# Kernel tuning notes

Measured on AMD Instinct MI355X. Metric: run time of the kernel, lower is better.

Reference implementation:

```python
import jax, jax.numpy as jnp
import numpy as np

NEG_SLOPE = 0.2  # PyG GATConv default leaky_relu slope


def segment_softmax(logits, seg, num_segments):
    # logits: [E, H], seg: [E] destination node ids
    m = jax.ops.segment_max(logits, seg, num_segments=num_segments)
    m = jnp.where(jnp.isfinite(m), m, 0.0)  # empty segments
    e = jnp.exp(logits - m[seg])
    s = jax.ops.segment_sum(e, seg, num_segments=num_segments)
    return e / (s[seg] + 1e-16)


def gat_conv(x, src, dst, W, att_src, att_dst, bias, heads, out_ch, concat, num_nodes):
    # x: [N, F_in], W: [F_in, heads*out_ch], att_*: [heads, out_ch]
    h = (x @ W).reshape(num_nodes, heads, out_ch)            # [N, H, C]
    a_src = jnp.sum(h * att_src, axis=-1)                    # [N, H]
    a_dst = jnp.sum(h * att_dst, axis=-1)                    # [N, H]
    logits = jax.nn.leaky_relu(a_src[src] + a_dst[dst], NEG_SLOPE)  # [E, H]
    alpha = segment_softmax(logits, dst, num_nodes)          # [E, H]
    msg = h[src] * alpha[..., None]                          # [E, H, C]
    out = jax.ops.segment_sum(msg, dst, num_segments=num_nodes)  # [N, H, C]
    out = out.reshape(num_nodes, heads * out_ch) if concat else out.mean(axis=1)
    return out + bias


def setup_inputs() -> dict:
    key = jax.random.key(0)
    ks = jax.random.split(key, 12)
    N, E = 50000, 800000
    F_in, Hd, H, F_out = 256, 128, 2, 64

    def glorot(k, shape):
        fan = shape[0] + shape[-1]
        return jax.random.normal(k, shape, dtype=jnp.float32) * jnp.sqrt(2.0 / fan)

    x = jax.random.normal(ks[0], (N, F_in), dtype=jnp.float32)
    edge_index = jax.random.randint(ks[1], (2, E), 0, N, dtype=jnp.int32)
    return {
        "x": x,
        "edge_index": edge_index,
        "W1": glorot(ks[2], (F_in, H * Hd)),
        "att_src1": glorot(ks[3], (H, Hd)),
        "att_dst1": glorot(ks[4], (H, Hd)),
        "b1": jnp.zeros((H * Hd,), dtype=jnp.float32),
        "W2": glorot(ks[5], (H * Hd, F_out)),
        "att_src2": glorot(ks[6], (1, F_out)),
        "att_dst2": glorot(ks[7], (1, F_out)),
        "b2": jnp.zeros((F_out,), dtype=jnp.float32),
    }


def reference(x, edge_index, W1, att_src1, att_dst1, b1, W2, att_src2, att_dst2, b2):
    N = x.shape[0]
    # PyG GATConv default: add self loops
    ar = jnp.arange(N, dtype=edge_index.dtype)
    src = jnp.concatenate([edge_index[0], ar])
    dst = jnp.concatenate([edge_index[1], ar])
    # dropout layers are identity in eval mode
    h = gat_conv(x, src, dst, W1, att_src1, att_dst1, b1,
                 heads=2, out_ch=128, concat=True, num_nodes=N)
    h = jax.nn.elu(h)
    out = gat_conv(h, src, dst, W2, att_src2, att_dst2, b2,
                   heads=1, out_ch=64, concat=False, num_nodes=N)
    return jax.nn.log_softmax(out, axis=1)
```

## Files before the change

### kernel.cpp

```cpp
#include <hip/hip_runtime.h>
#include <hip/hip_bf16.h>

typedef unsigned short u16;
typedef short bf8_t __attribute__((ext_vector_type(8)));
typedef float f32x4 __attribute__((ext_vector_type(4)));

__device__ inline u16 f2bf(float f) {
  unsigned u = __float_as_uint(f);
  u += 0x7FFFu + ((u >> 16) & 1u);
  return (u16)(u >> 16);
}
__device__ inline float bf2f(u16 h) { return __uint_as_float(((unsigned)h) << 16); }
__device__ inline float bflo(unsigned u) { return __uint_as_float(u << 16); }
__device__ inline float bfhi(unsigned u) { return __uint_as_float(u & 0xffff0000u); }

__global__ void prep_kernel(const int* __restrict__ ei, int E, int N,
                            int* __restrict__ counts,
                            const float* __restrict__ W1, const float* __restrict__ W2,
                            u16* __restrict__ W1T, u16* __restrict__ W2T, int nbc) {
  if ((int)blockIdx.x < nbc) {
    int e = blockIdx.x * 256 + threadIdx.x;
    int Et = E + N;
    if (e < Et) {
      int d = (e < E) ? ei[E + e] : (e - E);
      atomicAdd(&counts[d], 1);
    }
  } else {
    int idx = (blockIdx.x - nbc) * 256 + threadIdx.x;
    if (idx < 256 * 256) {
      int m = idx / 256, k = idx % 256;
      W1T[idx] = f2bf(W1[(size_t)k * 256 + m]);
    } else if (idx < 256 * 256 + 64 * 256) {
      int i = idx - 256 * 256;
      int m = i / 256, k = i % 256;
      W2T[i] = f2bf(W2[(size_t)k * 64 + m]);
    }
  }
}

template<int BM, int BN, int BK, int WM, int WN, bool AF32, int EPI>
__global__ __launch_bounds__(256) void mfma_gemm(const void* __restrict__ Ap,
                                                 const u16* __restrict__ Bt,
                                                 u16* __restrict__ C,
                                                 const float* __restrict__ att_s,
                                                 const float* __restrict__ att_d,
                                                 float* __restrict__ a_s,
                                                 float* __restrict__ a_d,
                                                 int N, int K) {
  constexpr int PAD = 8;
  __shared__ u16 As[BM][BK + PAD];
  __shared__ u16 Bs[BN][BK + PAD];
  const int tid = threadIdx.x;
  const int row0 = blockIdx.x * BM;
  const int w = tid >> 6, lane = tid & 63;
  const int wr = (w / (BN / WN)) * WM;
  const int wc = (w % (BN / WN)) * WN;
  constexpr int MF = WM / 16, NF = WN / 16;
  constexpr int CPR = BK / 8;
  f32x4 acc[MF][NF] = {};

  for (int k0 = 0; k0 < K; k0 += BK) {
    constexpr int ACH = BM * CPR;
#pragma unroll
    for (int c = 0; c < ACH; c += 256) {
      int cc = c + tid;
      int r = cc / CPR, kc = cc % CPR;
      int row = row0 + r;
      if (AF32) {
        const float* A = (const float*)Ap;
        float4 v0 = make_float4(0.f, 0.f, 0.f, 0.f), v1 = v0;
        if (row < N) {
          const float* p = A + (size_t)row * K + k0 + kc * 8;
          v0 = *(const float4*)p;
          v1 = *(const float4*)(p + 4);
        }
        union { __hip_bfloat162 h[4]; uint4 u; } cv;
        cv.h[0] = __float22bfloat162_rn(make_float2(v0.x, v0.y));
        cv.h[1] = __float22bfloat162_rn(make_float2(v0.z, v0.w));
        cv.h[2] = __float22bfloat162_rn(make_float2(v1.x, v1.y));
        cv.h[3] = __float22bfloat162_rn(make_float2(v1.z, v1.w));
        *(uint4*)&As[r][kc * 8] = cv.u;
      } else {
        const u16* A = (const u16*)Ap;
        uint4 v = make_uint4(0, 0, 0, 0);
        if (row < N) v = *(const uint4*)(A + (size_t)row * K + k0 + kc * 8);
        *(uint4*)&As[r][kc * 8] = v;
      }
    }
    constexpr int BCH = BN * CPR;
#pragma unroll
    for (int c = 0; c < BCH; c += 256) {
      int cc = c + tid;
      int r = cc / CPR, kc = cc % CPR;
      *(uint4*)&Bs[r][kc * 8] = *(const uint4*)(Bt + (size_t)r * K + k0 + kc * 8);
    }
    __syncthreads();
    const int lr = lane & 15, lk = (lane >> 4) * 8;
#pragma unroll
    for (int kk = 0; kk < BK; kk += 32) {
      bf8_t a[MF], b[NF];
#pragma unroll
      for (int mi = 0; mi < MF; ++mi) a[mi] = *(bf8_t*)&As[wr + mi * 16 + lr][kk + lk];
#pragma unroll
      for (int ni = 0; ni < NF; ++ni) b[ni] = *(bf8_t*)&Bs[wc + ni * 16 + lr][kk + lk];
#pragma unroll
      for (int mi = 0; mi < MF; ++mi)
#pragma unroll
        for (int ni = 0; ni < NF; ++ni)
          acc[mi][ni] = __builtin_amdgcn_mfma_f32_16x16x32_bf16(a[mi], b[ni], acc[mi][ni], 0, 0, 0);
    }
    __syncthreads();
  }
#pragma unroll
  for (int mi = 0; mi < MF; ++mi)
#pragma unroll
    for (int ni = 0; ni < NF; ++ni)
#pragma unroll
      for (int r = 0; r < 4; ++r) {
        int row = row0 + wr + mi * 16 + (lane >> 4) * 4 + r;
        int col = wc + ni * 16 + (lane & 15);
        if (row < N) C[(size_t)row * BN + col] = f2bf(acc[mi][ni][r]);
      }

  if (EPI == 1) {
    __shared__ float sm_s[4][64];
    __shared__ float sm_d[4][64];
    float asl[NF], adl[NF];
#pragma unroll
    for (int ni = 0; ni < NF; ++ni) {
      asl[ni] = att_s[wc + ni * 16 + (lane & 15)];
      adl[ni] = att_d[wc + ni * 16 + (lane & 15)];
    }
#pragma unroll
    for (int mi = 0; mi < MF; ++mi)
#pragma unroll
      for (int r = 0; r < 4; ++r) {
        float ps = 0.f, pd = 0.f;
#pragma unroll
        for (int ni = 0; ni < NF; ++ni) {
          float c = acc[mi][ni][r];
          ps += c * asl[ni];
          pd += c * adl[ni];
        }
#pragma unroll
        for (int o = 1; o < 16; o <<= 1) {
          ps += __shfl_xor(ps, o);
          pd += __shfl_xor(pd, o);
        }
        if ((lane & 15) == 0) {
          int row = mi * 16 + (lane >> 4) * 4 + r;
          sm_s[w][row] = ps;
          sm_d[w][row] = pd;
        }
      }
    __syncthreads();
    if (tid < 128) {
      int row = tid & 63, head = tid >> 6;
      int grow = row0 + row;
      if (grow < N) {
        a_s[grow * 2 + head] = sm_s[head * 2 + 0][row] + sm_s[head * 2 + 1][row];
        a_d[grow * 2 + head] = sm_d[head * 2 + 0][row] + sm_d[head * 2 + 1][row];
      }
    }
  } else if (EPI == 2) {
    float asl[NF], adl[NF];
#pragma unroll
    for (int ni = 0; ni < NF; ++ni) {
      asl[ni] = att_s[ni * 16 + (lane & 15)];
      adl[ni] = att_d[ni * 16 + (lane & 15)];
    }
#pragma unroll
    for (int mi = 0; mi < MF; ++mi)
#pragma unroll
      for (int r = 0; r < 4; ++r) {
        float ps = 0.f, pd = 0.f;
#pragma unroll
        for (int ni = 0; ni < NF; ++ni) {
          float c = acc[mi][ni][r];
          ps += c * asl[ni];
          pd += c * adl[ni];
        }
#pragma unroll
        for (int o = 1; o < 16; o <<= 1) {
          ps += __shfl_xor(ps, o);
          pd += __shfl_xor(pd, o);
        }
        int row = row0 + wr + mi * 16 + (lane >> 4) * 4 + r;
        if ((lane & 15) == 0 && row < N) {
          a_s[row] = ps;
          a_d[row] = pd;
        }
      }
  }
}

__global__ void block_scan_kernel(const int* __restrict__ counts, int* __restrict__ offsets,
                                  int* __restrict__ bsums, int N) {
  __shared__ int sm[256];
  int tid = threadIdx.x;
  int gid = blockIdx.x * 256 + tid;
  int v = (gid < N) ? counts[gid] : 0;
  int val = v;
  sm[tid] = val;
  __syncthreads();
  for (int off = 1; off < 256; off <<= 1) {
    int o = (tid >= off) ? sm[tid - off] : 0;
    __syncthreads();
    val += o;
    sm[tid] = val;
    __syncthreads();
  }
  if (gid < N) offsets[gid] = val - v;
  if (tid == 255) bsums[blockIdx.x] = val;
}

__global__ void scan_sums_kernel(int* __restrict__ bsums, int* __restrict__ offsets,
                                 int nb, int N) {
  __shared__ int sm[1024];
  int tid = threadIdx.x;
  int v = (tid < nb) ? bsums[tid] : 0;
  int val = v;
  sm[tid] = val;
  __syncthreads();
  for (int off = 1; off < 1024; off <<= 1) {
    int o = (tid >= off) ? sm[tid - off] : 0;
    __syncthreads();
    val += o;
    sm[tid] = val;
    __syncthreads();
  }
  if (tid < nb) bsums[tid] = val - v;
  if (tid == 1023) offsets[N] = val;
}

__global__ void add_base_kernel(int* __restrict__ offsets, int* __restrict__ cursor,
                                const int* __restrict__ bsums, int N) {
  int gid = blockIdx.x * 256 + threadIdx.x;
  if (gid >= N) return;
  int o = offsets[gid] + bsums[blockIdx.x];
  offsets[gid] = o;
  cursor[gid] = o;
}

__global__ void scatter_kernel(const int* __restrict__ ei, int E, int N,
                               int* __restrict__ cursor, int* __restrict__ csr_src) {
  int e = blockIdx.x * blockDim.x + threadIdx.x;
  int Et = E + N;
  if (e >= Et) return;
  int s, d;
  if (e < E) { s = ei[e]; d = ei[E + e]; }
  else       { s = d = e - E; }
  int pos = atomicAdd(&cursor[d], 1);
  csr_src[pos] = s;
}

__global__ void agg1_kernel(const u16* __restrict__ H1, const int* __restrict__ offsets,
                            const int* __restrict__ csr_src,
                            const float* __restrict__ a_src, const float* __restrict__ a_dst,
                            const float* __restrict__ b1, u16* __restrict__ out, int N) {
  __shared__ int4 meta[4][64];
  int wv = threadIdx.x >> 6;
  int lane = threadIdx.x & 63;
  int node = blockIdx.x * 4 + wv;
  if (node >= N) return;
  int off = offsets[node];
  int deg = offsets[node + 1] - off;
  float ad0 = a_dst[node * 2 + 0];
  float ad1 = a_dst[node * 2 + 1];
  bool hi = lane >= 32;
  const char* H1c = (const char*)H1;
  const unsigned loff = (unsigned)(lane * 8);
  float4 acc = make_float4(0.f, 0.f, 0.f, 0.f);
  float den = 0.f;
  const int4* mw = meta[wv];

  auto proc = [&](int4 m) {
    float w = hi ? __int_as_float(m.z) : __int_as_float(m.y);
    uint2 u = *(const uint2*)(H1c + (((unsigned)m.x << 9) + loff));
    den += w;
    acc.x += w * bflo(u.x);
    acc.y += w * bfhi(u.x);
    acc.z += w * bflo(u.y);
    acc.w += w * bfhi(u.y);
  };

  for (int base = 0; base < deg; base += 64) {
    int i = base + lane;
    if (i < deg) {
      int s = csr_src[off + i];
      float l0 = a_src[s * 2 + 0] + ad0;
      float l1 = a_src[s * 2 + 1] + ad1;
      l0 = l0 > 0.f ? l0 : 0.2f * l0;
      l1 = l1 > 0.f ? l1 : 0.2f * l1;
      meta[wv][lane] = make_int4(s, __float_as_int(__expf(l0)), __float_as_int(__expf(l1)), 0);
    }
    int cnt = min(64, deg - base);
    int j = 0;
    for (; j + 4 <= cnt; j += 4) {
      int4 m0 = mw[j], m1 = mw[j + 1], m2 = mw[j + 2], m3 = mw[j + 3];
      proc(m0); proc(m1); proc(m2); proc(m3);
    }
    for (; j < cnt; ++j) proc(mw[j]);
  }
  float inv = 1.f / (den + 1e-16f);
  float4 bb = *(const float4*)(b1 + lane * 4);
  float o0 = acc.x * inv + bb.x;
  float o1 = acc.y * inv + bb.y;
  float o2 = acc.z * inv + bb.z;
  float o3 = acc.w * inv + bb.w;
  o0 = o0 > 0.f ? o0 : expm1f(o0);
  o1 = o1 > 0.f ? o1 : expm1f(o1);
  o2 = o2 > 0.f ? o2 : expm1f(o2);
  o3 = o3 > 0.f ? o3 : expm1f(o3);
  uint2 ov;
  ov.x = (unsigned)f2bf(o0) | ((unsigned)f2bf(o1) << 16);
  ov.y = (unsigned)f2bf(o2) | ((unsigned)f2bf(o3) << 16);
  *(uint2*)(out + (size_t)node * 256 + lane * 4) = ov;
}

__global__ void agg2_kernel(const u16* __restrict__ H2, const int* __restrict__ offsets,
                            const int* __restrict__ csr_src,
                            const float* __restrict__ a_src, const float* __restrict__ a_dst,
                            const float* __restrict__ b2, float* __restrict__ out, int N) {
  __shared__ int2 meta[4][64];
  int wv = threadIdx.x >> 6;
  int lane = threadIdx.x & 63;
  int node = blockIdx.x * 4 + wv;
  if (node >= N) return;
  int off = offsets[node];
  int deg = offsets[node + 1] - off;
  float ad = a_dst[node];
  const int grp = lane >> 3;
  const int l3 = lane & 7;
  const char* H2c = (const char*)H2;
  const unsigned loff = (unsigned)(l3 * 16);
  float acc[8] = {0.f, 0.f, 0.f, 0.f, 0.f, 0.f, 0.f, 0.f};
  float den = 0.f;
  const int2* mw = meta[wv];

  auto proc = [&](int jj) {
    int2 m = mw[jj];
    float w = __int_as_float(m.y);
    uint4 u = *(const uint4*)(H2c + (((unsigned)m.x << 7) + loff));
    den += w;
    acc[0] += w * bflo(u.x); acc[1] += w * bfhi(u.x);
    acc[2] += w * bflo(u.y); acc[3] += w * bfhi(u.y);
    acc[4] += w * bflo(u.z); acc[5] += w * bfhi(u.z);
    acc[6] += w * bflo(u.w); acc[7] += w * bfhi(u.w);
  };

  for (int base = 0; base < deg; base += 64) {
    int i = base + lane;
    if (i < deg) {
      int s = csr_src[off + i];
      float l = a_src[s] + ad;
      l = l > 0.f ? l : 0.2f * l;
      meta[wv][lane] = make_int2(s, __float_as_int(__expf(l)));
    }
    int cnt = min(64, deg - base);
    int j = 0;
    for (; j + 16 <= cnt; j += 16) { proc(j + grp); proc(j + 8 + grp); }
    for (; j + 8 <= cnt; j += 8) proc(j + grp);
    int r = cnt - j;
    if (r > 0 && grp < r) proc(j + grp);
  }
#pragma unroll
  for (int k = 0; k < 8; ++k) {
    acc[k] += __shfl_xor(acc[k], 8);
    acc[k] += __shfl_xor(acc[k], 16);
    acc[k] += __shfl_xor(acc[k], 32);
  }
  den += __shfl_xor(den, 8);
  den += __shfl_xor(den, 16);
  den += __shfl_xor(den, 32);

  float inv = 1.f / (den + 1e-16f);
  float4 b01 = *(const float4*)(b2 + l3 * 8);
  float4 b23 = *(const float4*)(b2 + l3 * 8 + 4);
  float bb[8] = {b01.x, b01.y, b01.z, b01.w, b23.x, b23.y, b23.z, b23.w};
  float v[8];
#pragma unroll
  for (int k = 0; k < 8; ++k) v[k] = acc[k] * inv + bb[k];
  float m = v[0];
#pragma unroll
  for (int k = 1; k < 8; ++k) m = fmaxf(m, v[k]);
  m = fmaxf(m, __shfl_xor(m, 1));
  m = fmaxf(m, __shfl_xor(m, 2));
  m = fmaxf(m, __shfl_xor(m, 4));
  float sum = 0.f;
#pragma unroll
  for (int k = 0; k < 8; ++k) sum += __expf(v[k] - m);
  sum += __shfl_xor(sum, 1);
  sum += __shfl_xor(sum, 2);
  sum += __shfl_xor(sum, 4);
  float ls = m + logf(sum);
  if (lane < 8) {
    float4 o0 = make_float4(v[0] - ls, v[1] - ls, v[2] - ls, v[3] - ls);
    float4 o1 = make_float4(v[4] - ls, v[5] - ls, v[6] - ls, v[7] - ls);
    *(float4*)(out + (size_t)node * 64 + l3 * 8) = o0;
    *(float4*)(out + (size_t)node * 64 + l3 * 8 + 4) = o1;
  }
}

extern "C" void kernel_launch(void* const* d_in, const int* in_sizes, int n_in,
                              void* d_out, int out_size, void* d_ws, size_t ws_size,
                              hipStream_t stream) {
  const float* x   = (const float*)d_in[0];
  const int*   ei  = (const int*)d_in[1];
  const float* W1  = (const float*)d_in[2];
  const float* as1 = (const float*)d_in[3];
  const float* ad1 = (const float*)d_in[4];
  const float* b1  = (const float*)d_in[5];
  const float* W2  = (const float*)d_in[6];
  const float* as2 = (const float*)d_in[7];
  const float* ad2 = (const float*)d_in[8];
  const float* b2  = (const float*)d_in[9];
  float* out = (float*)d_out;

  const int N  = in_sizes[0] / 256;
  const int E  = in_sizes[1] / 2;
  const int Et = E + N;
  const int nb = (N + 255) / 256;
  const int nbc = (Et + 255) / 256;
  const int nbt = (256 * 256 + 64 * 256 + 255) / 256;

  char* p = (char*)d_ws;
  auto alloc = [&](size_t bytes) -> char* {
    char* r = p;
    p += (bytes + 255) & ~(size_t)255;
    return r;
  };
  u16* H1b     = (u16*)alloc((size_t)N * 256 * 2);
  u16* h1act   = (u16*)alloc((size_t)N * 256 * 2);
  u16* H2b     = (u16*)alloc((size_t)N * 64 * 2);
  u16* W1T     = (u16*)alloc((size_t)256 * 256 * 2);
  u16* W2T     = (u16*)alloc((size_t)64 * 256 * 2);
  float* a_src1 = (float*)alloc((size_t)N * 2 * 4);
  float* a_dst1 = (float*)alloc((size_t)N * 2 * 4);
  float* a_src2 = (float*)alloc((size_t)N * 4);
  float* a_dst2 = (float*)alloc((size_t)N * 4);
  int* counts   = (int*)alloc((size_t)N * 4);
  int* offsets  = (int*)alloc((size_t)(N + 1) * 4);
  int* cursor   = (int*)alloc((size_t)N * 4);
  int* bsums    = (int*)alloc((size_t)1024 * 4);
  int* csr_src  = (int*)alloc((size_t)Et * 4);

  const int tb = 256;

  hipMemsetAsync(counts, 0, (size_t)N * 4, stream);
  prep_kernel<<<nbc + nbt, tb, 0, stream>>>(ei, E, N, counts, W1, W2, W1T, W2T, nbc);
  block_scan_kernel<<<nb, 256, 0, stream>>>(counts, offsets, bsums, N);
  scan_sums_kernel<<<1, 1024, 0, stream>>>(bsums, offsets, nb, N);
  add_base_kernel<<<nb, 256, 0, stream>>>(offsets, cursor, bsums, N);
  scatter_kernel<<<(Et + tb - 1) / tb, tb, 0, stream>>>(ei, E, N, cursor, csr_src);

  mfma_gemm<64, 256, 64, 64, 64, true, 1><<<(N + 63) / 64, 256, 0, stream>>>(
      x, W1T, H1b, as1, ad1, a_src1, a_dst1, N, 256);
  agg1_kernel<<<(N + 3) / 4, 256, 0, stream>>>(H1b, offsets, csr_src, a_src1, a_dst1, b1,
                                               h1act, N);

  mfma_gemm<128, 64, 64, 32, 64, false, 2><<<(N + 127) / 128, 256, 0, stream>>>(
      h1act, W2T, H2b, as2, ad2, a_src2, a_dst2, N, 256);
  agg2_kernel<<<(N + 3) / 4, 256, 0, stream>>>(H2b, offsets, csr_src, a_src2, a_dst2, b2,
                                               out, N);
}
```

Baseline: 234.9 us.

## Fuse CSR construction into one cooperative kernel and shrink GEMM K-tile

Replaces the memset, the prep kernel, the three scan kernels and the scatter kernel with one cooperative kernel. It uses grid-wide syncs between the count, scan, base-add and scatter phases, with weight transposition folded into the first phase. The goal is to remove several launches and their inter-kernel gaps, at the price of grid.sync overhead and only 256 persistent blocks doing the edge atomics. The scan assumes N fits in 256x256 threads. Both GEMMs also drop BK from 64 to 32, trading fewer LDS bytes and possibly higher occupancy for more K-loop iterations.

Result: slower. 367.3 us (+56.4%).

```diff
diff --git a/kernel.cpp b/kernel.cpp
--- a/kernel.cpp
+++ b/kernel.cpp
@@ -1,5 +1,8 @@
 #include <hip/hip_runtime.h>
 #include <hip/hip_bf16.h>
+#include <hip/hip_cooperative_groups.h>
+
+namespace cg = cooperative_groups;
 
 typedef unsigned short u16;
 typedef short bf8_t __attribute__((ext_vector_type(8)));
@@ -14,27 +17,81 @@
 __device__ inline float bflo(unsigned u) { return __uint_as_float(u << 16); }
 __device__ inline float bfhi(unsigned u) { return __uint_as_float(u & 0xffff0000u); }
 
-__global__ void prep_kernel(const int* __restrict__ ei, int E, int N,
-                            int* __restrict__ counts,
-                            const float* __restrict__ W1, const float* __restrict__ W2,
-                            u16* __restrict__ W1T, u16* __restrict__ W2T, int nbc) {
-  if ((int)blockIdx.x < nbc) {
-    int e = blockIdx.x * 256 + threadIdx.x;
-    int Et = E + N;
-    if (e < Et) {
-      int d = (e < E) ? ei[E + e] : (e - E);
-      atomicAdd(&counts[d], 1);
-    }
-  } else {
-    int idx = (blockIdx.x - nbc) * 256 + threadIdx.x;
-    if (idx < 256 * 256) {
-      int m = idx / 256, k = idx % 256;
-      W1T[idx] = f2bf(W1[(size_t)k * 256 + m]);
-    } else if (idx < 256 * 256 + 64 * 256) {
-      int i = idx - 256 * 256;
-      int m = i / 256, k = i % 256;
-      W2T[i] = f2bf(W2[(size_t)k * 64 + m]);
-    }
+__global__ void csr_build_kernel(const int* __restrict__ ei, int E, int N,
+                                 const float* __restrict__ W1, const float* __restrict__ W2,
+                                 u16* __restrict__ W1T, u16* __restrict__ W2T,
+                                 int* __restrict__ counts, int* __restrict__ offsets,
+                                 int* __restrict__ cursor, int* __restrict__ bsums,
+                                 int* __restrict__ csr_src) {
+  cg::grid_group grid = cg::this_grid();
+  __shared__ int sm[256];
+  const int tid = threadIdx.x, bid = blockIdx.x;
+  const int gsz = gridDim.x * 256;
+  const int g = bid * 256 + tid;
+  const int Et = E + N;
+
+  for (int i = g; i < N; i += gsz) counts[i] = 0;
+  for (int i = g; i < 256 * 256; i += gsz) {
+    int m = i >> 8, k = i & 255;
+    W1T[i] = f2bf(W1[k * 256 + m]);
+  }
+  for (int i = g; i < 64 * 256; i += gsz) {
+    int m = i >> 8, k = i & 255;
+    W2T[i] = f2bf(W2[k * 64 + m]);
+  }
+  grid.sync();
+
+  for (int e = g; e < Et; e += gsz) {
+    int d = (e < E) ? ei[E + e] : (e - E);
+    atomicAdd(&counts[d], 1);
+  }
+  grid.sync();
+
+  int v = (g < N) ? counts[g] : 0;
+  int val = v;
+  sm[tid] = val;
+  __syncthreads();
+  for (int off = 1; off < 256; off <<= 1) {
+    int o = (tid >= off) ? sm[tid - off] : 0;
+    __syncthreads();
+    val += o;
+    sm[tid] = val;
+    __syncthreads();
+  }
+  if (g < N) offsets[g] = val - v;
+  if (tid == 255) bsums[bid] = val;
+  grid.sync();
+
+  if (bid == 0) {
+    int b = bsums[tid];
+    int bv = b;
+    sm[tid] = bv;
+    __syncthreads();
+    for (int off = 1; off < 256; off <<= 1) {
+      int o = (tid >= off) ? sm[tid - off] : 0;
+      __syncthreads();
+      bv += o;
+      sm[tid] = bv;
+      __syncthreads();
+    }
+    bsums[tid] = bv - b;
+    if (tid == 255) offsets[N] = bv;
+  }
+  grid.sync();
+
+  if (g < N) {
+    int o = offsets[g] + bsums[bid];
+    offsets[g] = o;
+    cursor[g] = o;
+  }
+  grid.sync();
+
+  for (int e = g; e < Et; e += gsz) {
+    int s, d;
+    if (e < E) { s = ei[e]; d = ei[E + e]; }
+    else       { s = d = e - E; }
+    int pos = atomicAdd(&cursor[d], 1);
+    csr_src[pos] = s;
   }
 }
 
@@ -194,66 +251,6 @@
   }
 }
 
-__global__ void block_scan_kernel(const int* __restrict__ counts, int* __restrict__ offsets,
-                                  int* __restrict__ bsums, int N) {
-  __shared__ int sm[256];
-  int tid = threadIdx.x;
-  int gid = blockIdx.x * 256 + tid;
-  int v = (gid < N) ? counts[gid] : 0;
-  int val = v;
-  sm[tid] = val;
-  __syncthreads();
-  for (int off = 1; off < 256; off <<= 1) {
-    int o = (tid >= off) ? sm[tid - off] : 0;
-    __syncthreads();
-    val += o;
-    sm[tid] = val;
-    __syncthreads();
-  }
-  if (gid < N) offsets[gid] = val - v;
-  if (tid == 255) bsums[blockIdx.x] = val;
-}
-
-__global__ void scan_sums_kernel(int* __restrict__ bsums, int* __restrict__ offsets,
-                                 int nb, int N) {
-  __shared__ int sm[1024];
-  int tid = threadIdx.x;
-  int v = (tid < nb) ? bsums[tid] : 0;
-  int val = v;
-  sm[tid] = val;
-  __syncthreads();
-  for (int off = 1; off < 1024; off <<= 1) {
-    int o = (tid >= off) ? sm[tid - off] : 0;
-    __syncthreads();
-    val += o;
-    sm[tid] = val;
-    __syncthreads();
-  }
-  if (tid < nb) bsums[tid] = val - v;
-  if (tid == 1023) offsets[N] = val;
-}
-
-__global__ void add_base_kernel(int* __restrict__ offsets, int* __restrict__ cursor,
-                                const int* __restrict__ bsums, int N) {
-  int gid = blockIdx.x * 256 + threadIdx.x;
-  if (gid >= N) return;
-  int o = offsets[gid] + bsums[blockIdx.x];
-  offsets[gid] = o;
-  cursor[gid] = o;
-}
-
-__global__ void scatter_kernel(const int* __restrict__ ei, int E, int N,
-                               int* __restrict__ cursor, int* __restrict__ csr_src) {
-  int e = blockIdx.x * blockDim.x + threadIdx.x;
-  int Et = E + N;
-  if (e >= Et) return;
-  int s, d;
-  if (e < E) { s = ei[e]; d = ei[E + e]; }
-  else       { s = d = e - E; }
-  int pos = atomicAdd(&cursor[d], 1);
-  csr_src[pos] = s;
-}
-
 __global__ void agg1_kernel(const u16* __restrict__ H1, const int* __restrict__ offsets,
                             const int* __restrict__ csr_src,
                             const float* __restrict__ a_src, const float* __restrict__ a_dst,
@@ -417,12 +414,9 @@
   const float* b2  = (const float*)d_in[9];
   float* out = (float*)d_out;
 
-  const int N  = in_sizes[0] / 256;
-  const int E  = in_sizes[1] / 2;
+  int N  = in_sizes[0] / 256;
+  int E  = in_sizes[1] / 2;
   const int Et = E + N;
-  const int nb = (N + 255) / 256;
-  const int nbc = (Et + 255) / 256;
-  const int nbt = (256 * 256 + 64 * 256 + 255) / 256;
 
   char* p = (char*)d_ws;
   auto alloc = [&](size_t bytes) -> char* {
@@ -445,21 +439,20 @@
   int* bsums    = (int*)alloc((size_t)1024 * 4);
   int* csr_src  = (int*)alloc((size_t)Et * 4);
 
-  const int tb = 256;
-
-  hipMemsetAsync(counts, 0, (size_t)N * 4, stream);
-  prep_kernel<<<nbc + nbt, tb, 0, stream>>>(ei, E, N, counts, W1, W2, W1T, W2T, nbc);
-  block_scan_kernel<<<nb, 256, 0, stream>>>(counts, offsets, bsums, N);
-  scan_sums_kernel<<<1, 1024, 0, stream>>>(bsums, offsets, nb, N);
-  add_base_kernel<<<nb, 256, 0, stream>>>(offsets, cursor, bsums, N);
-  scatter_kernel<<<(Et + tb - 1) / tb, tb, 0, stream>>>(ei, E, N, cursor, csr_src);
-
-  mfma_gemm<64, 256, 64, 64, 64, true, 1><<<(N + 63) / 64, 256, 0, stream>>>(
+  {
+    void* args[] = {(void*)&ei, (void*)&E, (void*)&N, (void*)&W1, (void*)&W2,
+                    (void*)&W1T, (void*)&W2T, (void*)&counts, (void*)&offsets,
+                    (void*)&cursor, (void*)&bsums, (void*)&csr_src};
+    hipLaunchCooperativeKernel((void*)csr_build_kernel, dim3(256), dim3(256),
+                               args, 0, stream);
+  }
+
+  mfma_gemm<64, 256, 32, 64, 64, true, 1><<<(N + 63) / 64, 256, 0, stream>>>(
       x, W1T, H1b, as1, ad1, a_src1, a_dst1, N, 256);
   agg1_kernel<<<(N + 3) / 4, 256, 0, stream>>>(H1b, offsets, csr_src, a_src1, a_dst1, b1,
                                                h1act, N);
 
-  mfma_gemm<128, 64, 64, 32, 64, false, 2><<<(N + 127) / 128, 256, 0, stream>>>(
+  mfma_gemm<128, 64, 32, 32, 64, false, 2><<<(N + 127) / 128, 256, 0, stream>>>(
       h1act, W2T, H2b, as2, ad2, a_src2, a_dst2, N, 256);
   agg2_kernel<<<(N + 3) / 4, 256, 0, stream>>>(H2b, offsets, csr_src, a_src2, a_dst2, b2,
                                                out, N);
```

## Fuse scan into decoupled-lookback kernel and merge CSR scatter into GEMM1 launch

Applied to the files above, without the earlier changes.

Replaces the three-kernel prefix scan with a single-pass decoupled-lookback scan that also initializes cursors. The CSR scatter now runs as extra blocks appended to the first GEMM launch, so that work overlaps with the matrix multiply. GEMM BK shrinks from 64 to 32, which changes shared-memory footprint and loop count. The aim is fewer launches and less serialization. The cost is spin-waiting in the scan, which relies on earlier blocks being scheduled first.

Result: slower. 276.8 us (+17.9%).

```diff
diff --git a/kernel.cpp b/kernel.cpp
--- a/kernel.cpp
+++ b/kernel.cpp
@@ -28,14 +28,66 @@
   } else {
     int idx = (blockIdx.x - nbc) * 256 + threadIdx.x;
     if (idx < 256 * 256) {
-      int m = idx / 256, k = idx % 256;
-      W1T[idx] = f2bf(W1[(size_t)k * 256 + m]);
+      int m = idx >> 8, k = idx & 255;
+      W1T[idx] = f2bf(W1[k * 256 + m]);
     } else if (idx < 256 * 256 + 64 * 256) {
       int i = idx - 256 * 256;
-      int m = i / 256, k = i % 256;
-      W2T[i] = f2bf(W2[(size_t)k * 64 + m]);
-    }
-  }
+      int m = i >> 8, k = i & 255;
+      W2T[i] = f2bf(W2[k * 64 + m]);
+    }
+  }
+}
+
+__global__ void scan_kernel(const int* __restrict__ counts, int* __restrict__ offsets,
+                            int* __restrict__ cursor,
+                            unsigned long long* __restrict__ bstate, int N, int nb) {
+  __shared__ int sm[256];
+  __shared__ int base_sh;
+  const int tid = threadIdx.x, bid = blockIdx.x;
+  const int gid = bid * 256 + tid;
+  int v = (gid < N) ? counts[gid] : 0;
+  int val = v;
+  sm[tid] = val;
+  __syncthreads();
+  for (int off = 1; off < 256; off <<= 1) {
+    int o = (tid >= off) ? sm[tid - off] : 0;
+    __syncthreads();
+    val += o;
+    sm[tid] = val;
+    __syncthreads();
+  }
+  int total = sm[255];
+  if (tid == 0) {
+    if (bid == 0) {
+      __hip_atomic_store(&bstate[0], ((unsigned long long)(unsigned)total << 32) | 2ull,
+                         __ATOMIC_RELEASE, __HIP_MEMORY_SCOPE_AGENT);
+      base_sh = 0;
+    } else {
+      __hip_atomic_store(&bstate[bid], ((unsigned long long)(unsigned)total << 32) | 1ull,
+                         __ATOMIC_RELEASE, __HIP_MEMORY_SCOPE_AGENT);
+      int base = 0;
+      for (int pb = bid - 1; pb >= 0; --pb) {
+        unsigned long long st;
+        do {
+          st = __hip_atomic_load(&bstate[pb], __ATOMIC_ACQUIRE, __HIP_MEMORY_SCOPE_AGENT);
+        } while ((st & 3ull) == 0ull);
+        base += (int)(unsigned)(st >> 32);
+        if ((st & 3ull) == 2ull) break;
+      }
+      __hip_atomic_store(&bstate[bid],
+                         ((unsigned long long)(unsigned)(base + total) << 32) | 2ull,
+                         __ATOMIC_RELEASE, __HIP_MEMORY_SCOPE_AGENT);
+      base_sh = base;
+    }
+  }
+  __syncthreads();
+  int base = base_sh;
+  if (gid < N) {
+    int o = base + val - v;
+    offsets[gid] = o;
+    cursor[gid] = o;
+  }
+  if (bid == nb - 1 && tid == 255) offsets[N] = base + total;
 }
 
 template<int BM, int BN, int BK, int WM, int WN, bool AF32, int EPI>
@@ -46,7 +98,24 @@
                                                  const float* __restrict__ att_d,
                                                  float* __restrict__ a_s,
                                                  float* __restrict__ a_d,
-                                                 int N, int K) {
+                                                 int N, int K,
+                                                 const int* __restrict__ ei, int E,
+                                                 int* __restrict__ cursor,
+                                                 int* __restrict__ csr_src,
+                                                 int gemmBlocks) {
+  if (EPI == 1 && (int)blockIdx.x >= gemmBlocks) {
+    int e = ((int)blockIdx.x - gemmBlocks) * 256 + (int)threadIdx.x;
+    int Et = E + N;
+    if (e < Et) {
+      int s, d;
+      if (e < E) { s = ei[e]; d = ei[E + e]; }
+      else       { s = d = e - E; }
+      int pos = atomicAdd(&cursor[d], 1);
+      csr_src[pos] = s;
+    }
+    return;
+  }
+
   constexpr int PAD = 8;
   __shared__ u16 As[BM][BK + PAD];
   __shared__ u16 Bs[BN][BK + PAD];
@@ -96,19 +165,16 @@
     }
     __syncthreads();
     const int lr = lane & 15, lk = (lane >> 4) * 8;
-#pragma unroll
-    for (int kk = 0; kk < BK; kk += 32) {
-      bf8_t a[MF], b[NF];
-#pragma unroll
-      for (int mi = 0; mi < MF; ++mi) a[mi] = *(bf8_t*)&As[wr + mi * 16 + lr][kk + lk];
-#pragma unroll
-      for (int ni = 0; ni < NF; ++ni) b[ni] = *(bf8_t*)&Bs[wc + ni * 16 + lr][kk + lk];
-#pragma unroll
-      for (int mi = 0; mi < MF; ++mi)
-#pragma unroll
-        for (int ni = 0; ni < NF; ++ni)
-          acc[mi][ni] = __builtin_amdgcn_mfma_f32_16x16x32_bf16(a[mi], b[ni], acc[mi][ni], 0, 0, 0);
-    }
+    bf8_t a[MF], b[NF];
+#pragma unroll
+    for (int mi = 0; mi < MF; ++mi) a[mi] = *(bf8_t*)&As[wr + mi * 16 + lr][lk];
+#pragma unroll
+    for (int ni = 0; ni < NF; ++ni) b[ni] = *(bf8_t*)&Bs[wc + ni * 16 + lr][lk];
+#pragma unroll
+    for (int mi = 0; mi < MF; ++mi)
+#pragma unroll
+      for (int ni = 0; ni < NF; ++ni)
+        acc[mi][ni] = __builtin_amdgcn_mfma_f32_16x16x32_bf16(a[mi], b[ni], acc[mi][ni], 0, 0, 0);
     __syncthreads();
   }
 #pragma unroll
@@ -192,66 +258,6 @@
         }
       }
   }
-}
-
-__global__ void block_scan_kernel(const int* __restrict__ counts, int* __restrict__ offsets,
-                                  int* __restrict__ bsums, int N) {
-  __shared__ int sm[256];
-  int tid = threadIdx.x;
-  int gid = blockIdx.x * 256 + tid;
-  int v = (gid < N) ? counts[gid] : 0;
-  int val = v;
-  sm[tid] = val;
-  __syncthreads();
-  for (int off = 1; off < 256; off <<= 1) {
-    int o = (tid >= off) ? sm[tid - off] : 0;
-    __syncthreads();
-    val += o;
-    sm[tid] = val;
-    __syncthreads();
-  }
-  if (gid < N) offsets[gid] = val - v;
-  if (tid == 255) bsums[blockIdx.x] = val;
-}
-
-__global__ void scan_sums_kernel(int* __restrict__ bsums, int* __restrict__ offsets,
-                                 int nb, int N) {
-  __shared__ int sm[1024];
-  int tid = threadIdx.x;
-  int v = (tid < nb) ? bsums[tid] : 0;
-  int val = v;
-  sm[tid] = val;
-  __syncthreads();
-  for (int off = 1; off < 1024; off <<= 1) {
-    int o = (tid >= off) ? sm[tid - off] : 0;
-    __syncthreads();
-    val += o;
-    sm[tid] = val;
-    __syncthreads();
-  }
-  if (tid < nb) bsums[tid] = val - v;
-  if (tid == 1023) offsets[N] = val;
-}
-
-__global__ void add_base_kernel(int* __restrict__ offsets, int* __restrict__ cursor,
-                                const int* __restrict__ bsums, int N) {
-  int gid = blockIdx.x * 256 + threadIdx.x;
-  if (gid >= N) return;
-  int o = offsets[gid] + bsums[blockIdx.x];
-  offsets[gid] = o;
-  cursor[gid] = o;
-}
-
-__global__ void scatter_kernel(const int* __restrict__ ei, int E, int N,
-                               int* __restrict__ cursor, int* __restrict__ csr_src) {
-  int e = blockIdx.x * blockDim.x + threadIdx.x;
-  int Et = E + N;
-  if (e >= Et) return;
-  int s, d;
-  if (e < E) { s = ei[e]; d = ei[E + e]; }
-  else       { s = d = e - E; }
-  int pos = atomicAdd(&cursor[d], 1);
-  csr_src[pos] = s;
 }
 
 __global__ void agg1_kernel(const u16* __restrict__ H1, const int* __restrict__ offsets,
@@ -420,9 +426,10 @@
   const int N  = in_sizes[0] / 256;
   const int E  = in_sizes[1] / 2;
   const int Et = E + N;
-  const int nb = (N + 255) / 256;
+  const int nb  = (N + 255) / 256;
   const int nbc = (Et + 255) / 256;
   const int nbt = (256 * 256 + 64 * 256 + 255) / 256;
+  const int sb  = (Et + 255) / 256;
 
   char* p = (char*)d_ws;
   auto alloc = [&](size_t bytes) -> char* {
@@ -440,27 +447,29 @@
   float* a_src2 = (float*)alloc((size_t)N * 4);
   float* a_dst2 = (float*)alloc((size_t)N * 4);
   int* counts   = (int*)alloc((size_t)N * 4);
+  unsigned long long* bstate = (unsigned long long*)alloc((size_t)1024 * 8);
   int* offsets  = (int*)alloc((size_t)(N + 1) * 4);
   int* cursor   = (int*)alloc((size_t)N * 4);
-  int* bsums    = (int*)alloc((size_t)1024 * 4);
   int* csr_src  = (int*)alloc((size_t)Et * 4);
 
   const int tb = 256;
 
-  hipMemsetAsync(counts, 0, (size_t)N * 4, stream);
+  size_t zlen = (char*)offsets - (char*)counts;
+  hipMemsetAsync(counts, 0, zlen, stream);
+
   prep_kernel<<<nbc + nbt, tb, 0, stream>>>(ei, E, N, counts, W1, W2, W1T, W2T, nbc);
-  block_scan_kernel<<<nb, 256, 0, stream>>>(counts, offsets, bsums, N);
-  scan_sums_kernel<<<1, 1024, 0, stream>>>(bsums, offsets, nb, N);
-  add_base_kernel<<<nb, 256, 0, stream>>>(offsets, cursor, bsums, N);
-  scatter_kernel<<<(Et + tb - 1) / tb, tb, 0, stream>>>(ei, E, N, cursor, csr_src);
-
-  mfma_gemm<64, 256, 64, 64, 64, true, 1><<<(N + 63) / 64, 256, 0, stream>>>(
-      x, W1T, H1b, as1, ad1, a_src1, a_dst1, N, 256);
-  agg1_kernel<<<(N + 3) / 4, 256, 0, stream>>>(H1b, offsets, csr_src, a_src1, a_dst1, b1,
-                                               h1act, N);
-
-  mfma_gemm<128, 64, 64, 32, 64, false, 2><<<(N + 127) / 128, 256, 0, stream>>>(
-      h1act, W2T, H2b, as2, ad2, a_src2, a_dst2, N, 256);
-  agg2_kernel<<<(N + 3) / 4, 256, 0, stream>>>(H2b, offsets, csr_src, a_src2, a_dst2, b2,
-                                               out, N);
-}
+
+  scan_kernel<<<nb, tb, 0, stream>>>(counts, offsets, cursor, bstate, N, nb);
+
+  const int g1 = (N + 63) / 64;
+  mfma_gemm<64, 256, 32, 64, 64, true, 1><<<g1 + sb, tb, 0, stream>>>(
+      x, W1T, H1b, as1, ad1, a_src1, a_dst1, N, 256, ei, E, cursor, csr_src, g1);
+  agg1_kernel<<<(N + 3) / 4, tb, 0, stream>>>(H1b, offsets, csr_src, a_src1, a_dst1, b1,
+                                              h1act, N);
+
+  const int g2 = (N + 127) / 128;
+  mfma_gemm<128, 64, 32, 32, 64, false, 2><<<g2, tb, 0, stream>>>(
+      h1act, W2T, H2b, as2, ad2, a_src2, a_dst2, N, 256, nullptr, 0, nullptr, nullptr, g2);
+  agg2_kernel<<<(N + 3) / 4, tb, 0, stream>>>(H2b, offsets, csr_src, a_src2, a_dst2, b2,
+                                              out, N);
+}
```
